# Kernel tuning notes

Hardware: AMD Instinct MI355X
Metric: run time of the kernel (lower is better)

Reference implementation:

```python
import jax, jax.numpy as jnp
import numpy as np

DIM = 256
HEADS = 8
WS = 7  # window_size
EPS = 1e-5


def dwconv1d(x, w, b):
    # x: (B, Cg, L); w: (Cg, 1, k); depthwise (groups=Cg), 'same' padding for odd k
    k = w.shape[-1]
    p = k // 2
    y = jax.lax.conv_general_dilated(
        x, w, window_strides=(1,), padding=[(p, p)],
        dimension_numbers=('NCH', 'OIH', 'NCH'),
        feature_group_count=x.shape[1])
    return y + b[None, :, None]


def group_norm(x, scale, bias, groups):
    # x: (B, C, *spatial); normalize over (C//groups, *spatial) per group
    B, C = x.shape[0], x.shape[1]
    xg = x.reshape(B, groups, -1)
    mean = xg.mean(-1, keepdims=True)
    var = xg.var(-1, keepdims=True)
    xn = ((xg - mean) * jax.lax.rsqrt(var + EPS)).reshape(x.shape)
    bshape = (1, C) + (1,) * (x.ndim - 2)
    return xn * scale.reshape(bshape) + bias.reshape(bshape)


def setup_inputs() -> dict:
    key = jax.random.key(0)
    ks = jax.random.split(key, 16)
    gc = DIM // 4
    d = {"x": jax.random.normal(ks[0], (32, DIM, 56, 56), dtype=jnp.float32)}
    for i, k in enumerate([3, 5, 7, 9]):
        d[f"w_dwc{k}"] = jax.random.normal(ks[1 + i], (gc, 1, k), dtype=jnp.float32) * (1.0 / np.sqrt(k))
        d[f"b_dwc{k}"] = jax.random.normal(ks[5 + i], (gc,), dtype=jnp.float32) * 0.02
    d["norm_h_scale"] = jnp.ones((DIM,), jnp.float32)
    d["norm_h_bias"] = jnp.zeros((DIM,), jnp.float32)
    d["norm_w_scale"] = jnp.ones((DIM,), jnp.float32)
    d["norm_w_bias"] = jnp.zeros((DIM,), jnp.float32)
    d["norm_scale"] = jnp.ones((DIM,), jnp.float32)
    d["norm_bias"] = jnp.zeros((DIM,), jnp.float32)
    d["q_w"] = jax.random.normal(ks[9], (DIM,), dtype=jnp.float32)
    d["k_w"] = jax.random.normal(ks[10], (DIM,), dtype=jnp.float32)
    d["v_w"] = jax.random.normal(ks[11], (DIM,), dtype=jnp.float32)
    return d


def reference(x, w_dwc3, b_dwc3, w_dwc5, b_dwc5, w_dwc7, b_dwc7, w_dwc9, b_dwc9,
              norm_h_scale, norm_h_bias, norm_w_scale, norm_w_bias,
              norm_scale, norm_bias, q_w, k_w, v_w):
    b, c, h, w = x.shape
    head_dim = c // HEADS

    def sa_branch(xm, scale, bias):
        # xm: (B, C, L) -> sigmoid(GroupNorm4(concat of 4 depthwise convs))
        p0, p1, p2, p3 = jnp.split(xm, 4, axis=1)
        y = jnp.concatenate([
            dwconv1d(p0, w_dwc3, b_dwc3),
            dwconv1d(p1, w_dwc5, b_dwc5),
            dwconv1d(p2, w_dwc7, b_dwc7),
            dwconv1d(p3, w_dwc9, b_dwc9)], axis=1)
        return jax.nn.sigmoid(group_norm(y, scale, bias, 4))

    x_h_attn = sa_branch(x.mean(axis=3), norm_h_scale, norm_h_bias)[:, :, :, None]  # (B,C,H,1)
    x_w_attn = sa_branch(x.mean(axis=2), norm_w_scale, norm_w_bias)[:, :, None, :]  # (B,C,1,W)
    xg = x * x_h_attn * x_w_attn

    # AvgPool2d(WS, stride=WS)
    hs, ws_ = h // WS, w // WS
    y = xg.reshape(b, c, hs, WS, ws_, WS).mean(axis=(3, 5))  # (B,C,hs,ws)
    y = group_norm(y, norm_scale, norm_bias, 1)

    n = hs * ws_
    q = (y * q_w[None, :, None, None]).reshape(b, HEADS, head_dim, n)
    k = (y * k_w[None, :, None, None]).reshape(b, HEADS, head_dim, n)
    v = (y * v_w[None, :, None, None]).reshape(b, HEADS, head_dim, n)

    attn = jnp.einsum('bhdn,bhen->bhde', q, k) * (head_dim ** -0.5)
    attn = jax.nn.softmax(attn, axis=-1)
    out = jnp.einsum('bhde,bhen->bhdn', attn, v)  # (B,H,hd,n)

    ca = jax.nn.sigmoid(out.reshape(b, c, n).mean(axis=-1))[:, :, None, None]  # (B,C,1,1)
    return ca * xg
```

## Files before the change

kernel.cpp:

```cpp
#include <hip/hip_runtime.h>
#include <cstdint>
#include <cstddef>

#define NB 32
#define NC 256
#define HW 56
#define PLANE (HW*HW)
#define NPLANE (NB*NC)
#define NHEADS 8
#define HDIM 32
#define NPOOL 64
#define EPSV 1e-5f

__global__ __launch_bounds__(256) void k_means(const float* __restrict__ x,
                                               float* __restrict__ hm,
                                               float* __restrict__ wm) {
    int plane = blockIdx.x;
    __shared__ float sm[PLANE];
    const float4* xp = (const float4*)(x + (size_t)plane * PLANE);
    float4* smp = (float4*)sm;
    int t = threadIdx.x;
    for (int f = t; f < PLANE / 4; f += 256) smp[f] = xp[f];
    __syncthreads();
    if (t < 56) {
        float s = 0.f;
#pragma unroll
        for (int j = 0; j < 56; ++j) {
            int jj = j + t; if (jj >= 56) jj -= 56;
            s += sm[t * 56 + jj];
        }
        hm[(size_t)plane * 56 + t] = s * (1.f / 56.f);
    } else if (t >= 64 && t < 120) {
        int cc = t - 64;
        float s = 0.f;
#pragma unroll
        for (int i = 0; i < 56; ++i) s += sm[i * 56 + cc];
        wm[(size_t)plane * 56 + cc] = s * (1.f / 56.f);
    }
}

__global__ __launch_bounds__(256) void k_branch(
    const float* __restrict__ hm, const float* __restrict__ wm,
    const float* __restrict__ w3, const float* __restrict__ b3,
    const float* __restrict__ w5, const float* __restrict__ b5,
    const float* __restrict__ w7, const float* __restrict__ b7,
    const float* __restrict__ w9, const float* __restrict__ b9,
    const float* __restrict__ hsc, const float* __restrict__ hbi,
    const float* __restrict__ wsc, const float* __restrict__ wbi,
    float* __restrict__ hattn, float* __restrict__ wattn) {
    int mode = blockIdx.x & 1;
    int b = blockIdx.x >> 1;
    const float* src = (mode == 0 ? hm : wm) + (size_t)b * NC * 56;
    const float* scale = (mode == 0 ? hsc : wsc);
    const float* bias = (mode == 0 ? hbi : wbi);
    float* dst = (mode == 0 ? hattn : wattn) + (size_t)b * NC * 56;

    int c = threadIdx.x;
    int g = c >> 6, cc = c & 63;

    float wc[9];
#pragma unroll
    for (int i = 0; i < 9; ++i) wc[i] = 0.f;
    float bb = 0.f;
    if (g == 0) {
#pragma unroll
        for (int t = 0; t < 3; ++t) wc[3 + t] = w3[cc * 3 + t];
        bb = b3[cc];
    } else if (g == 1) {
#pragma unroll
        for (int t = 0; t < 5; ++t) wc[2 + t] = w5[cc * 5 + t];
        bb = b5[cc];
    } else if (g == 2) {
#pragma unroll
        for (int t = 0; t < 7; ++t) wc[1 + t] = w7[cc * 7 + t];
        bb = b7[cc];
    } else {
#pragma unroll
        for (int t = 0; t < 9; ++t) wc[t] = w9[cc * 9 + t];
        bb = b9[cc];
    }

    float xpad[64];
#pragma unroll
    for (int i = 0; i < 64; ++i) xpad[i] = 0.f;
#pragma unroll
    for (int i = 0; i < 56; ++i) xpad[i + 4] = src[c * 56 + i];

    float y[56];
    float s1 = 0.f, s2 = 0.f;
#pragma unroll
    for (int i = 0; i < 56; ++i) {
        float a = bb;
#pragma unroll
        for (int d = 0; d < 9; ++d) a += wc[d] * xpad[i + d];
        y[i] = a;
        s1 += a;
        s2 += a * a;
    }
#pragma unroll
    for (int off = 32; off >= 1; off >>= 1) {
        s1 += __shfl_xor(s1, off);
        s2 += __shfl_xor(s2, off);
    }
    float mean = s1 * (1.f / 3584.f);
    float var = s2 * (1.f / 3584.f) - mean * mean;
    float rstd = rsqrtf(var + EPSV);
    float scv = scale[c];
    float a_lin = scv * rstd;
    float b_lin = bias[c] - mean * rstd * scv;
#pragma unroll
    for (int i = 0; i < 56; ++i) {
        float v = y[i] * a_lin + b_lin;
        dst[c * 56 + i] = 1.f / (1.f + expf(-v));
    }
}

__global__ __launch_bounds__(256) void k_pool(const float* __restrict__ x,
                                              const float* __restrict__ hattn,
                                              const float* __restrict__ wattn,
                                              float* __restrict__ ypool) {
    int plane = blockIdx.x;
    __shared__ float sm[PLANE];
    __shared__ float ha[56], wa[56];
    const float4* xp = (const float4*)(x + (size_t)plane * PLANE);
    float4* smp = (float4*)sm;
    int t = threadIdx.x;
    for (int f = t; f < PLANE / 4; f += 256) smp[f] = xp[f];
    if (t < 56) ha[t] = hattn[(size_t)plane * 56 + t];
    else if (t >= 64 && t < 120) wa[t - 64] = wattn[(size_t)plane * 56 + (t - 64)];
    __syncthreads();
    if (t < 64) {
        int i = t >> 3, j = t & 7;
        float s = 0.f;
#pragma unroll
        for (int dh = 0; dh < 7; ++dh) {
            float hv = ha[7 * i + dh];
            float r = 0.f;
#pragma unroll
            for (int dw = 0; dw < 7; ++dw)
                r += sm[(7 * i + dh) * 56 + 7 * j + dw] * wa[7 * j + dw];
            s += hv * r;
        }
        ypool[(size_t)plane * NPOOL + t] = s * (1.f / 49.f);
    }
}

__global__ __launch_bounds__(256) void k_stats(const float* __restrict__ ypool,
                                               float* __restrict__ stats) {
    int b = blockIdx.x;
    const float* p = ypool + (size_t)b * NC * NPOOL;
    int t = threadIdx.x;
    float s1 = 0.f, s2 = 0.f;
    for (int i = t; i < NC * NPOOL; i += 256) {
        float v = p[i];
        s1 += v;
        s2 += v * v;
    }
#pragma unroll
    for (int off = 32; off >= 1; off >>= 1) {
        s1 += __shfl_xor(s1, off);
        s2 += __shfl_xor(s2, off);
    }
    __shared__ float a1[4], a2[4];
    int w = t >> 6;
    if ((t & 63) == 0) { a1[w] = s1; a2[w] = s2; }
    __syncthreads();
    if (t == 0) {
        float t1 = a1[0] + a1[1] + a1[2] + a1[3];
        float t2 = a2[0] + a2[1] + a2[2] + a2[3];
        float mean = t1 * (1.f / (NC * NPOOL));
        float var = t2 * (1.f / (NC * NPOOL)) - mean * mean;
        stats[2 * b] = mean;
        stats[2 * b + 1] = rsqrtf(var + EPSV);
    }
}

__global__ __launch_bounds__(64) void k_attn(const float* __restrict__ ypool,
                                             const float* __restrict__ stats,
                                             const float* __restrict__ nsc,
                                             const float* __restrict__ nbi,
                                             const float* __restrict__ qw,
                                             const float* __restrict__ kw,
                                             const float* __restrict__ vw,
                                             float* __restrict__ ca) {
    int bh = blockIdx.x;
    int b = bh >> 3, h = bh & 7;
    float mean = stats[2 * b], rstd = stats[2 * b + 1];
    __shared__ float yn[32][65];
    __shared__ float ybar[32];
    __shared__ float G[32][33];
    int l = threadIdx.x;
    const float* base = ypool + ((size_t)b * NC + h * HDIM) * NPOOL;
#pragma unroll
    for (int m = 0; m < 32; ++m) {
        int idx = l + 64 * m;
        int d = idx >> 6, p = idx & 63;
        int ch = h * HDIM + d;
        float v = base[idx];
        yn[d][p] = (v - mean) * rstd * nsc[ch] + nbi[ch];
    }
    __syncthreads();
    if (l < 32) {
        float s = 0.f;
#pragma unroll
        for (int p = 0; p < 64; ++p) s += yn[l][p];
        ybar[l] = s * (1.f / 64.f);
    }
    __syncthreads();
#pragma unroll
    for (int m = 0; m < 16; ++m) {
        int idx = l + 64 * m;
        int d = idx >> 5, e = idx & 31;
        float s = 0.f;
#pragma unroll
        for (int p = 0; p < 64; ++p) s += yn[d][p] * yn[e][p];
        G[d][e] = s;
    }
    __syncthreads();
    if (l < 32) {
        int d = l, cd = h * HDIM + d;
        float qs = qw[cd] * 0.17677669529663687f;
        float a[32];
        float mx = -1e30f;
#pragma unroll
        for (int e = 0; e < 32; ++e) {
            a[e] = G[d][e] * qs * kw[h * HDIM + e];
            mx = fmaxf(mx, a[e]);
        }
        float sum = 0.f;
#pragma unroll
        for (int e = 0; e < 32; ++e) {
            a[e] = expf(a[e] - mx);
            sum += a[e];
        }
        float o = 0.f;
#pragma unroll
        for (int e = 0; e < 32; ++e) o += a[e] * vw[h * HDIM + e] * ybar[e];
        o /= sum;
        ca[b * NC + cd] = 1.f / (1.f + expf(-o));
    }
}

__global__ __launch_bounds__(256) void k_final(const float* __restrict__ x,
                                               const float* __restrict__ hattn,
                                               const float* __restrict__ wattn,
                                               const float* __restrict__ ca,
                                               float* __restrict__ out) {
    int plane = blockIdx.x;
    __shared__ float hv[56], wv[56];
    int t = threadIdx.x;
    float cav = ca[plane];
    if (t < 56) hv[t] = hattn[(size_t)plane * 56 + t] * cav;
    else if (t >= 64 && t < 120) wv[t - 64] = wattn[(size_t)plane * 56 + (t - 64)];
    __syncthreads();
    const float4* xp = (const float4*)(x + (size_t)plane * PLANE);
    float4* op = (float4*)(out + (size_t)plane * PLANE);
    for (int f = t; f < PLANE / 4; f += 256) {
        int r = f / 14;
        int s0 = (f - r * 14) * 4;
        float4 v = xp[f];
        float hf = hv[r];
        v.x *= hf * wv[s0];
        v.y *= hf * wv[s0 + 1];
        v.z *= hf * wv[s0 + 2];
        v.w *= hf * wv[s0 + 3];
        op[f] = v;
    }
}

extern "C" void kernel_launch(void* const* d_in, const int* in_sizes, int n_in,
                              void* d_out, int out_size, void* d_ws, size_t ws_size,
                              hipStream_t stream) {
    const float* x   = (const float*)d_in[0];
    const float* w3  = (const float*)d_in[1];
    const float* b3  = (const float*)d_in[2];
    const float* w5  = (const float*)d_in[3];
    const float* b5  = (const float*)d_in[4];
    const float* w7  = (const float*)d_in[5];
    const float* b7  = (const float*)d_in[6];
    const float* w9  = (const float*)d_in[7];
    const float* b9  = (const float*)d_in[8];
    const float* hsc = (const float*)d_in[9];
    const float* hbi = (const float*)d_in[10];
    const float* wsc = (const float*)d_in[11];
    const float* wbi = (const float*)d_in[12];
    const float* nsc = (const float*)d_in[13];
    const float* nbi = (const float*)d_in[14];
    const float* qw  = (const float*)d_in[15];
    const float* kw  = (const float*)d_in[16];
    const float* vw  = (const float*)d_in[17];
    float* out = (float*)d_out;

    float* ws    = (float*)d_ws;
    float* hm    = ws;
    float* wm    = hm + (size_t)NPLANE * 56;
    float* hattn = wm + (size_t)NPLANE * 56;
    float* wattn = hattn + (size_t)NPLANE * 56;
    float* ypool = wattn + (size_t)NPLANE * 56;
    float* stats = ypool + (size_t)NPLANE * NPOOL;
    float* cav   = stats + 64;

    k_means<<<NPLANE, 256, 0, stream>>>(x, hm, wm);
    k_branch<<<2 * NB, 256, 0, stream>>>(hm, wm, w3, b3, w5, b5, w7, b7, w9, b9,
                                         hsc, hbi, wsc, wbi, hattn, wattn);
    k_pool<<<NPLANE, 256, 0, stream>>>(x, hattn, wattn, ypool);
    k_stats<<<NB, 256, 0, stream>>>(ypool, stats);
    k_attn<<<NB * NHEADS, 64, 0, stream>>>(ypool, stats, nsc, nbi, qw, kw, vw, cav);
    k_final<<<NPLANE, 256, 0, stream>>>(x, hattn, wattn, cav, out);
}
```

Before: 294.9 us.

## Parallelize row/col means, stage branch I/O via LDS, fuse stats into attention

k_means now uses 224 threads, with four lanes per row and column combined by shuffles, instead of 112 serial threads. k_branch stages its input and output through padded shared memory with coalesced float4 accesses and recomputes the convolution rather than holding a 56-element register array. The separate k_stats kernel is removed and each k_attn block recomputes the per-batch GroupNorm statistics itself. The cost is redundant reads of the ypool batch slice, eight times per batch, and the convolution being computed twice.

```diff
diff --git a/kernel.cpp b/kernel.cpp
--- a/kernel.cpp
+++ b/kernel.cpp
@@ -22,20 +22,20 @@
     int t = threadIdx.x;
     for (int f = t; f < PLANE / 4; f += 256) smp[f] = xp[f];
     __syncthreads();
-    if (t < 56) {
+    if (t < 224) {
+        int a = t >> 2, q = t & 3;
         float s = 0.f;
 #pragma unroll
-        for (int j = 0; j < 56; ++j) {
-            int jj = j + t; if (jj >= 56) jj -= 56;
-            s += sm[t * 56 + jj];
-        }
-        hm[(size_t)plane * 56 + t] = s * (1.f / 56.f);
-    } else if (t >= 64 && t < 120) {
-        int cc = t - 64;
-        float s = 0.f;
-#pragma unroll
-        for (int i = 0; i < 56; ++i) s += sm[i * 56 + cc];
-        wm[(size_t)plane * 56 + cc] = s * (1.f / 56.f);
+        for (int i = 0; i < 14; ++i) s += sm[a * 56 + q * 14 + i];
+        s += __shfl_xor(s, 1);
+        s += __shfl_xor(s, 2);
+        if (q == 0) hm[(size_t)plane * 56 + a] = s * (1.f / 56.f);
+        float s2 = 0.f;
+#pragma unroll
+        for (int i = 0; i < 14; ++i) s2 += sm[(q * 14 + i) * 56 + a];
+        s2 += __shfl_xor(s2, 1);
+        s2 += __shfl_xor(s2, 2);
+        if (q == 0) wm[(size_t)plane * 56 + a] = s2 * (1.f / 56.f);
     }
 }
 
@@ -55,7 +55,21 @@
     const float* bias = (mode == 0 ? hbi : wbi);
     float* dst = (mode == 0 ? hattn : wattn) + (size_t)b * NC * 56;
 
-    int c = threadIdx.x;
+    __shared__ float sm[NC * 57];
+    int t = threadIdx.x;
+
+    const float4* sp = (const float4*)src;
+#pragma unroll
+    for (int k = 0; k < 14; ++k) {
+        int f = t + 256 * k;
+        float4 v = sp[f];
+        int c = f / 14, r = f - c * 14;
+        float* d = &sm[c * 57 + r * 4];
+        d[0] = v.x; d[1] = v.y; d[2] = v.z; d[3] = v.w;
+    }
+    __syncthreads();
+
+    int c = t;
     int g = c >> 6, cc = c & 63;
 
     float wc[9];
@@ -64,36 +78,35 @@
     float bb = 0.f;
     if (g == 0) {
 #pragma unroll
-        for (int t = 0; t < 3; ++t) wc[3 + t] = w3[cc * 3 + t];
+        for (int q = 0; q < 3; ++q) wc[3 + q] = w3[cc * 3 + q];
         bb = b3[cc];
     } else if (g == 1) {
 #pragma unroll
-        for (int t = 0; t < 5; ++t) wc[2 + t] = w5[cc * 5 + t];
+        for (int q = 0; q < 5; ++q) wc[2 + q] = w5[cc * 5 + q];
         bb = b5[cc];
     } else if (g == 2) {
 #pragma unroll
-        for (int t = 0; t < 7; ++t) wc[1 + t] = w7[cc * 7 + t];
+        for (int q = 0; q < 7; ++q) wc[1 + q] = w7[cc * 7 + q];
         bb = b7[cc];
     } else {
 #pragma unroll
-        for (int t = 0; t < 9; ++t) wc[t] = w9[cc * 9 + t];
+        for (int q = 0; q < 9; ++q) wc[q] = w9[cc * 9 + q];
         bb = b9[cc];
     }
 
-    float xpad[64];
-#pragma unroll
-    for (int i = 0; i < 64; ++i) xpad[i] = 0.f;
-#pragma unroll
-    for (int i = 0; i < 56; ++i) xpad[i + 4] = src[c * 56 + i];
-
-    float y[56];
+    float xv[56];
+#pragma unroll
+    for (int i = 0; i < 56; ++i) xv[i] = sm[c * 57 + i];
+
     float s1 = 0.f, s2 = 0.f;
 #pragma unroll
     for (int i = 0; i < 56; ++i) {
         float a = bb;
 #pragma unroll
-        for (int d = 0; d < 9; ++d) a += wc[d] * xpad[i + d];
-        y[i] = a;
+        for (int d = 0; d < 9; ++d) {
+            int j = i + d - 4;
+            if (j >= 0 && j < 56) a += wc[d] * xv[j];
+        }
         s1 += a;
         s2 += a * a;
     }
@@ -108,10 +121,27 @@
     float scv = scale[c];
     float a_lin = scv * rstd;
     float b_lin = bias[c] - mean * rstd * scv;
+
 #pragma unroll
     for (int i = 0; i < 56; ++i) {
-        float v = y[i] * a_lin + b_lin;
-        dst[c * 56 + i] = 1.f / (1.f + expf(-v));
+        float a = bb;
+#pragma unroll
+        for (int d = 0; d < 9; ++d) {
+            int j = i + d - 4;
+            if (j >= 0 && j < 56) a += wc[d] * xv[j];
+        }
+        float v = a * a_lin + b_lin;
+        sm[c * 57 + i] = 1.f / (1.f + expf(-v));
+    }
+    __syncthreads();
+
+    float4* dp = (float4*)dst;
+#pragma unroll
+    for (int k = 0; k < 14; ++k) {
+        int f = t + 256 * k;
+        int c2 = f / 14, r = f - c2 * 14;
+        const float* s = &sm[c2 * 57 + r * 4];
+        dp[f] = make_float4(s[0], s[1], s[2], s[3]);
     }
 }
 
@@ -145,38 +175,7 @@
     }
 }
 
-__global__ __launch_bounds__(256) void k_stats(const float* __restrict__ ypool,
-                                               float* __restrict__ stats) {
-    int b = blockIdx.x;
-    const float* p = ypool + (size_t)b * NC * NPOOL;
-    int t = threadIdx.x;
-    float s1 = 0.f, s2 = 0.f;
-    for (int i = t; i < NC * NPOOL; i += 256) {
-        float v = p[i];
-        s1 += v;
-        s2 += v * v;
-    }
-#pragma unroll
-    for (int off = 32; off >= 1; off >>= 1) {
-        s1 += __shfl_xor(s1, off);
-        s2 += __shfl_xor(s2, off);
-    }
-    __shared__ float a1[4], a2[4];
-    int w = t >> 6;
-    if ((t & 63) == 0) { a1[w] = s1; a2[w] = s2; }
-    __syncthreads();
-    if (t == 0) {
-        float t1 = a1[0] + a1[1] + a1[2] + a1[3];
-        float t2 = a2[0] + a2[1] + a2[2] + a2[3];
-        float mean = t1 * (1.f / (NC * NPOOL));
-        float var = t2 * (1.f / (NC * NPOOL)) - mean * mean;
-        stats[2 * b] = mean;
-        stats[2 * b + 1] = rsqrtf(var + EPSV);
-    }
-}
-
 __global__ __launch_bounds__(64) void k_attn(const float* __restrict__ ypool,
-                                             const float* __restrict__ stats,
                                              const float* __restrict__ nsc,
                                              const float* __restrict__ nbi,
                                              const float* __restrict__ qw,
@@ -185,11 +184,28 @@
                                              float* __restrict__ ca) {
     int bh = blockIdx.x;
     int b = bh >> 3, h = bh & 7;
-    float mean = stats[2 * b], rstd = stats[2 * b + 1];
+    int l = threadIdx.x;
+
+    const float4* bp = (const float4*)(ypool + (size_t)b * NC * NPOOL);
+    float s1 = 0.f, s2 = 0.f;
+#pragma unroll
+    for (int k = 0; k < 64; ++k) {
+        float4 v = bp[l + 64 * k];
+        s1 += v.x + v.y + v.z + v.w;
+        s2 += v.x * v.x + v.y * v.y + v.z * v.z + v.w * v.w;
+    }
+#pragma unroll
+    for (int off = 32; off >= 1; off >>= 1) {
+        s1 += __shfl_xor(s1, off);
+        s2 += __shfl_xor(s2, off);
+    }
+    float mean = s1 * (1.f / (NC * NPOOL));
+    float var = s2 * (1.f / (NC * NPOOL)) - mean * mean;
+    float rstd = rsqrtf(var + EPSV);
+
     __shared__ float yn[32][65];
     __shared__ float ybar[32];
     __shared__ float G[32][33];
-    int l = threadIdx.x;
     const float* base = ypool + ((size_t)b * NC + h * HDIM) * NPOOL;
 #pragma unroll
     for (int m = 0; m < 32; ++m) {
@@ -297,14 +313,12 @@
     float* hattn = wm + (size_t)NPLANE * 56;
     float* wattn = hattn + (size_t)NPLANE * 56;
     float* ypool = wattn + (size_t)NPLANE * 56;
-    float* stats = ypool + (size_t)NPLANE * NPOOL;
-    float* cav   = stats + 64;
+    float* cav   = ypool + (size_t)NPLANE * NPOOL;
 
     k_means<<<NPLANE, 256, 0, stream>>>(x, hm, wm);
     k_branch<<<2 * NB, 256, 0, stream>>>(hm, wm, w3, b3, w5, b5, w7, b7, w9, b9,
                                          hsc, hbi, wsc, wbi, hattn, wattn);
     k_pool<<<NPLANE, 256, 0, stream>>>(x, hattn, wattn, ypool);
-    k_stats<<<NB, 256, 0, stream>>>(ypool, stats);
-    k_attn<<<NB * NHEADS, 64, 0, stream>>>(ypool, stats, nsc, nbi, qw, kw, vw, cav);
+    k_attn<<<NB * NHEADS, 64, 0, stream>>>(ypool, nsc, nbi, qw, kw, vw, cav);
     k_final<<<NPLANE, 256, 0, stream>>>(x, hattn, wattn, cav, out);
 }
```

Result: faster. 285.8 us (-3.1%).
